# Optimization experiments

Measured on AMD Instinct MI355X. Metric: run time of the kernel, lower is better.

The kernel has to match this reference:

```python
import jax, jax.numpy as jnp
import numpy as np

CHUNK_SIZE = 64
EPS = 1e-6


def setup_inputs() -> dict:
    key = jax.random.key(0)
    ks = jax.random.split(key, 5)
    B, NH, S, DH = 2, 16, 4096, 64
    return {
        "q": jax.random.normal(ks[0], (B, NH, S, DH), dtype=jnp.float32),
        "k": jax.random.normal(ks[1], (B, NH, S, DH), dtype=jnp.float32),
        "v": jax.random.normal(ks[2], (B, NH, S, DH), dtype=jnp.float32),
        "igate_preact": jax.random.normal(ks[3], (B, NH, S), dtype=jnp.float32),
        "fgate_preact": jax.random.normal(ks[4], (B, NH, S), dtype=jnp.float32),
    }


def _mlstm_intra(q, k, v, ig, fg, chunk_size, eps):
    # q,k,v: [B,NH,S,DH]; ig,fg: [B,NH,S]
    B, NH, S, DH = q.shape
    L = chunk_size
    NC = S // L
    qc = q.reshape(B, NH, NC, L, DH)
    kc = k.reshape(B, NH, NC, L, DH)
    vc = v.reshape(B, NH, NC, L, DH)
    igc = ig.reshape(B, NH, NC, L)
    fgc = fg.reshape(B, NH, NC, L)

    # log forget gates and their within-chunk cumulative sums
    log_fg = jax.nn.log_sigmoid(fgc)                      # [B,NH,NC,L]
    log_fg_cum = jnp.cumsum(log_fg, axis=-1)              # [B,NH,NC,L]

    # gated decay matrix: logD[i,j] = sum_{t=j+1..i} log f_t + i_j  for j<=i
    log_fg_mat = log_fg_cum[..., :, None] - log_fg_cum[..., None, :]  # [B,NH,NC,L,L]
    log_D = log_fg_mat + igc[..., None, :]
    causal = jnp.tril(jnp.ones((L, L), dtype=bool))
    log_D = jnp.where(causal, log_D, -jnp.inf)

    # stabilizer (row-wise max)
    m = jnp.max(log_D, axis=-1)                           # [B,NH,NC,L]
    D = jnp.exp(log_D - m[..., None])                     # [B,NH,NC,L,L]

    # QK scores scaled, gated by decay matrix
    scale = 1.0 / jnp.sqrt(jnp.asarray(DH, dtype=q.dtype))
    scores = jnp.einsum("bncld,bncsd->bncls", qc, kc) * scale
    C = scores * D                                        # [B,NH,NC,L,L]

    # stabilized normalizer: max(|row sum|, exp(-m))
    n = jnp.maximum(jnp.abs(jnp.sum(C, axis=-1)), jnp.exp(-m))  # [B,NH,NC,L]
    h = jnp.einsum("bncls,bncsd->bncld", C, vc) / (n[..., None] + eps)
    return h.reshape(B, NH, S, DH)


def reference(q, k, v, igate_preact, fgate_preact):
    return _mlstm_intra(q, k, v, igate_preact, fgate_preact, CHUNK_SIZE, EPS)
```

## Files before the change

kernel.cpp:

```cpp
#include <hip/hip_runtime.h>
#include <hip/hip_bf16.h>
#include <math.h>

namespace {

typedef __bf16 bf16x8 __attribute__((ext_vector_type(8)));
typedef float f32x4 __attribute__((ext_vector_type(4)));

constexpr int L = 64;
constexpr int DH = 64;

__device__ __forceinline__ int kkey(int r) { return (r ^ (r >> 2)) & 7; }

__device__ __forceinline__ int swzV(int d, int j) {
  return d * 128 + ((((j >> 3) ^ kkey(d)) & 7) << 4) + (j & 7) * 2;
}
__device__ __forceinline__ int swzC(int r, int j) {
  return r * 128 + ((((j >> 3) ^ kkey(r)) & 7) << 4) + (j & 7) * 2;
}

__device__ __forceinline__ unsigned short bfbits(float f) {
  __bf16 h = (__bf16)f;
  return __builtin_bit_cast(unsigned short, h);
}
__device__ __forceinline__ __bf16 tobf(float f) { return (__bf16)f; }

__global__ __launch_bounds__(256) void mlstm_mfma(
    const float* __restrict__ q, const float* __restrict__ k,
    const float* __restrict__ v, const float* __restrict__ ig,
    const float* __restrict__ fg, float* __restrict__ out) {

  __shared__ __align__(16) char lds[8192 + 4 * 2048];
  __shared__ __align__(16) float ea_sh[64];
  __shared__ __align__(16) float eb_sh[64];
  __shared__ __align__(16) float em_sh[64];

  const int tid = threadIdx.x;
  const int w = tid >> 6;
  const int lane = tid & 63;
  const int m = lane & 15;
  const int g = lane >> 4;
  const size_t cbase = (size_t)blockIdx.x * (L * DH);
  const size_t gb = (size_t)blockIdx.x * L;

  const float4* v4 = (const float4*)(v + cbase);
  float4 vbuf[4];
#pragma unroll
  for (int it = 0; it < 4; ++it) vbuf[it] = v4[it * 256 + tid];

  float fgv = 0.f, igv = 0.f;
  if (w == 0) {
    fgv = fg[gb + lane];
    igv = ig[gb + lane];
  }

  bf16x8 qf[2];
#pragma unroll
  for (int kb = 0; kb < 2; ++kb) {
    const int off = (w * 16 + m) * 64 + kb * 32 + g * 8;
    const float4 q0 = *(const float4*)(q + cbase + off);
    const float4 q1 = *(const float4*)(q + cbase + off + 4);
    qf[kb] = bf16x8{tobf(q0.x), tobf(q0.y), tobf(q0.z), tobf(q0.w),
                    tobf(q1.x), tobf(q1.y), tobf(q1.z), tobf(q1.w)};
  }
  bf16x8 kf[4][2];
#pragma unroll
  for (int rb = 0; rb < 4; ++rb) {
    if (rb <= w) {
#pragma unroll
      for (int kb = 0; kb < 2; ++kb) {
        const int off = (rb * 16 + m) * 64 + kb * 32 + g * 8;
        const float4 k0 = *(const float4*)(k + cbase + off);
        const float4 k1 = *(const float4*)(k + cbase + off + 4);
        kf[rb][kb] = bf16x8{tobf(k0.x), tobf(k0.y), tobf(k0.z), tobf(k0.w),
                            tobf(k1.x), tobf(k1.y), tobf(k1.z), tobf(k1.w)};
      }
    }
  }

  if (w == 0) {
    const float lf = fminf(fgv, 0.f) - log1pf(__expf(-fabsf(fgv)));
    float cum = lf;
#pragma unroll
    for (int o = 1; o < 64; o <<= 1) {
      const float t = __shfl_up(cum, o, 64);
      if (lane >= o) cum += t;
    }
    const float a = igv - cum;
    float b = a;
#pragma unroll
    for (int o = 1; o < 64; o <<= 1) {
      const float t = __shfl_up(b, o, 64);
      if (lane >= o) b = fmaxf(b, t);
    }
    const float bmax = __shfl(b, 63, 64);
    ea_sh[lane] = 0.125f * __expf(a - bmax);
    eb_sh[lane] = __expf(bmax - b);
    em_sh[lane] = __expf(-(b + cum));
  }

  {
    unsigned short* vt = (unsigned short*)lds;
#pragma unroll
    for (int it = 0; it < 4; ++it) {
      const int idx = it * 256 + tid;
      const int j = idx >> 4;
      const int d0 = (idx & 15) * 4;
      vt[swzV(d0 + 0, j) >> 1] = bfbits(vbuf[it].x);
      vt[swzV(d0 + 1, j) >> 1] = bfbits(vbuf[it].y);
      vt[swzV(d0 + 2, j) >> 1] = bfbits(vbuf[it].z);
      vt[swzV(d0 + 3, j) >> 1] = bfbits(vbuf[it].w);
    }
  }

  __syncthreads();

  const int njb = (w >= 2) ? 2 : 1;
  bf16x8 vfr[4][2];
#pragma unroll
  for (int db = 0; db < 4; ++db)
#pragma unroll
    for (int jb = 0; jb < 2; ++jb)
      if (jb < njb)
        vfr[db][jb] =
            *(const bf16x8*)(lds + swzV(db * 16 + m, jb * 32 + g * 8));

  f32x4 st[4];
#pragma unroll
  for (int rb = 0; rb < 4; ++rb) {
    if (rb <= w) {
      f32x4 acc = {0.f, 0.f, 0.f, 0.f};
      acc = __builtin_amdgcn_mfma_f32_16x16x32_bf16(kf[rb][0], qf[0], acc, 0, 0, 0);
      acc = __builtin_amdgcn_mfma_f32_16x16x32_bf16(kf[rb][1], qf[1], acc, 0, 0, 0);
      st[rb] = acc;
    }
  }

  char* cw = lds + 8192 + w * 2048;
  const int i = w * 16 + m;
  const float ebv = eb_sh[i];
  float rs = 0.f;
  const int rbfill = w | 1;
#pragma unroll
  for (int rb = 0; rb < 4; ++rb) {
    if (rb <= rbfill) {
      unsigned long long wp = 0ull;
      if (rb <= w) {
        const float4 ea4 = *(const float4*)&ea_sh[rb * 16 + g * 4];
        const float eav[4] = {ea4.x, ea4.y, ea4.z, ea4.w};
#pragma unroll
        for (int e = 0; e < 4; ++e) {
          const int j = rb * 16 + g * 4 + e;
          const float val = (j <= i) ? st[rb][e] * eav[e] * ebv : 0.f;
          rs += val;
          wp |= (unsigned long long)bfbits(val) << (16 * e);
        }
      }
      *(unsigned long long*)(cw + swzC(m, rb * 16 + g * 4)) = wp;
    }
  }
  rs += __shfl_xor(rs, 16, 64);
  rs += __shfl_xor(rs, 32, 64);
  const float invv = 1.f / (fmaxf(fabsf(rs), em_sh[i]) + 1e-6f);

  const bf16x8 c0 = *(const bf16x8*)(cw + swzC(m, g * 8));
  f32x4 acc[4];
#pragma unroll
  for (int db = 0; db < 4; ++db) {
    f32x4 z = {0.f, 0.f, 0.f, 0.f};
    acc[db] = __builtin_amdgcn_mfma_f32_16x16x32_bf16(vfr[db][0], c0, z, 0, 0, 0);
  }
  if (w >= 2) {
    const bf16x8 c1 = *(const bf16x8*)(cw + swzC(m, 32 + g * 8));
#pragma unroll
    for (int db = 0; db < 4; ++db)
      acc[db] = __builtin_amdgcn_mfma_f32_16x16x32_bf16(vfr[db][1], c1, acc[db], 0, 0, 0);
  }

  float* op = out + cbase + i * 64 + g * 4;
#pragma unroll
  for (int db = 0; db < 4; ++db) {
    const f32x4 hv = acc[db];
    *(float4*)(op + db * 16) =
        make_float4(hv[0] * invv, hv[1] * invv, hv[2] * invv, hv[3] * invv);
  }
}

}

extern "C" void kernel_launch(void* const* d_in, const int* in_sizes, int n_in,
                              void* d_out, int out_size, void* d_ws,
                              size_t ws_size, hipStream_t stream) {
  const float* q = (const float*)d_in[0];
  const float* k = (const float*)d_in[1];
  const float* v = (const float*)d_in[2];
  const float* ig = (const float*)d_in[3];
  const float* fg = (const float*)d_in[4];
  float* out = (float*)d_out;

  const int total = in_sizes[0];
  const int nchunks = total / (L * DH);
  mlstm_mfma<<<dim3(nchunks), dim3(256), 0, stream>>>(q, k, v, ig, fg, out);
}
```

Before: 30.26 us.

## Remove block-wide sync by loading V fragments directly and computing gates per wave

Every wave now computes the gate scan redundantly and shares its per-row factors through lane shuffles instead of shared memory. V is loaded straight from global memory in fragment order, replacing the transposed LDS staging. Together these drop the block-wide __syncthreads and shrink LDS use, and launch bounds now request 4 blocks per CU. The cost is strided scalar global loads for V, redundant gate math in each wave, and more registers held for V values.

New measurement: 34.74 us. +14.8%, slower.

```diff
diff --git a/kernel.cpp b/kernel.cpp
--- a/kernel.cpp
+++ b/kernel.cpp
@@ -11,10 +11,6 @@
 constexpr int DH = 64;
 
 __device__ __forceinline__ int kkey(int r) { return (r ^ (r >> 2)) & 7; }
-
-__device__ __forceinline__ int swzV(int d, int j) {
-  return d * 128 + ((((j >> 3) ^ kkey(d)) & 7) << 4) + (j & 7) * 2;
-}
 __device__ __forceinline__ int swzC(int r, int j) {
   return r * 128 + ((((j >> 3) ^ kkey(r)) & 7) << 4) + (j & 7) * 2;
 }
@@ -25,15 +21,12 @@
 }
 __device__ __forceinline__ __bf16 tobf(float f) { return (__bf16)f; }
 
-__global__ __launch_bounds__(256) void mlstm_mfma(
+__global__ __launch_bounds__(256, 4) void mlstm_mfma(
     const float* __restrict__ q, const float* __restrict__ k,
     const float* __restrict__ v, const float* __restrict__ ig,
     const float* __restrict__ fg, float* __restrict__ out) {
 
-  __shared__ __align__(16) char lds[8192 + 4 * 2048];
-  __shared__ __align__(16) float ea_sh[64];
-  __shared__ __align__(16) float eb_sh[64];
-  __shared__ __align__(16) float em_sh[64];
+  __shared__ __align__(16) char lds[4 * 2048];
 
   const int tid = threadIdx.x;
   const int w = tid >> 6;
@@ -43,16 +36,21 @@
   const size_t cbase = (size_t)blockIdx.x * (L * DH);
   const size_t gb = (size_t)blockIdx.x * L;
 
-  const float4* v4 = (const float4*)(v + cbase);
-  float4 vbuf[4];
+  const float fgv = fg[gb + lane];
+  const float igv = ig[gb + lane];
+
+  const int njb = (w >= 2) ? 2 : 1;
+  float vtmp[4][2][8];
 #pragma unroll
-  for (int it = 0; it < 4; ++it) vbuf[it] = v4[it * 256 + tid];
-
-  float fgv = 0.f, igv = 0.f;
-  if (w == 0) {
-    fgv = fg[gb + lane];
-    igv = ig[gb + lane];
-  }
+  for (int db = 0; db < 4; ++db)
+#pragma unroll
+    for (int jb = 0; jb < 2; ++jb)
+      if (jb < njb) {
+        const float* vp =
+            v + cbase + (size_t)(jb * 32 + g * 8) * 64 + db * 16 + m;
+#pragma unroll
+        for (int t = 0; t < 8; ++t) vtmp[db][jb][t] = vp[t * 64];
+      }
 
   bf16x8 qf[2];
 #pragma unroll
@@ -78,7 +76,8 @@
     }
   }
 
-  if (w == 0) {
+  float ea, eb, em;
+  {
     const float lf = fminf(fgv, 0.f) - log1pf(__expf(-fabsf(fgv)));
     float cum = lf;
 #pragma unroll
@@ -94,36 +93,21 @@
       if (lane >= o) b = fmaxf(b, t);
     }
     const float bmax = __shfl(b, 63, 64);
-    ea_sh[lane] = 0.125f * __expf(a - bmax);
-    eb_sh[lane] = __expf(bmax - b);
-    em_sh[lane] = __expf(-(b + cum));
+    ea = 0.125f * __expf(a - bmax);
+    eb = __expf(bmax - b);
+    em = __expf(-(b + cum));
   }
 
-  {
-    unsigned short* vt = (unsigned short*)lds;
-#pragma unroll
-    for (int it = 0; it < 4; ++it) {
-      const int idx = it * 256 + tid;
-      const int j = idx >> 4;
-      const int d0 = (idx & 15) * 4;
-      vt[swzV(d0 + 0, j) >> 1] = bfbits(vbuf[it].x);
-      vt[swzV(d0 + 1, j) >> 1] = bfbits(vbuf[it].y);
-      vt[swzV(d0 + 2, j) >> 1] = bfbits(vbuf[it].z);
-      vt[swzV(d0 + 3, j) >> 1] = bfbits(vbuf[it].w);
-    }
-  }
-
-  __syncthreads();
-
-  const int njb = (w >= 2) ? 2 : 1;
   bf16x8 vfr[4][2];
 #pragma unroll
   for (int db = 0; db < 4; ++db)
 #pragma unroll
     for (int jb = 0; jb < 2; ++jb)
-      if (jb < njb)
-        vfr[db][jb] =
-            *(const bf16x8*)(lds + swzV(db * 16 + m, jb * 32 + g * 8));
+      if (jb < njb) {
+        const float* t = vtmp[db][jb];
+        vfr[db][jb] = bf16x8{tobf(t[0]), tobf(t[1]), tobf(t[2]), tobf(t[3]),
+                             tobf(t[4]), tobf(t[5]), tobf(t[6]), tobf(t[7])};
+      }
 
   f32x4 st[4];
 #pragma unroll
@@ -136,9 +120,10 @@
     }
   }
 
-  char* cw = lds + 8192 + w * 2048;
+  char* cw = lds + w * 2048;
   const int i = w * 16 + m;
-  const float ebv = eb_sh[i];
+  const float ebv = __shfl(eb, i, 64);
+  const float emv = __shfl(em, i, 64);
   float rs = 0.f;
   const int rbfill = w | 1;
 #pragma unroll
@@ -146,12 +131,11 @@
     if (rb <= rbfill) {
       unsigned long long wp = 0ull;
       if (rb <= w) {
-        const float4 ea4 = *(const float4*)&ea_sh[rb * 16 + g * 4];
-        const float eav[4] = {ea4.x, ea4.y, ea4.z, ea4.w};
 #pragma unroll
         for (int e = 0; e < 4; ++e) {
           const int j = rb * 16 + g * 4 + e;
-          const float val = (j <= i) ? st[rb][e] * eav[e] * ebv : 0.f;
+          const float eaj = __shfl(ea, j, 64);
+          const float val = (j <= i) ? st[rb][e] * eaj * ebv : 0.f;
           rs += val;
           wp |= (unsigned long long)bfbits(val) << (16 * e);
         }
@@ -161,7 +145,7 @@
   }
   rs += __shfl_xor(rs, 16, 64);
   rs += __shfl_xor(rs, 32, 64);
-  const float invv = 1.f / (fmaxf(fabsf(rs), em_sh[i]) + 1e-6f);
+  const float invv = 1.f / (fmaxf(fabsf(rs), emv) + 1e-6f);
 
   const bf16x8 c0 = *(const bf16x8*)(cw + swzC(m, g * 8));
   f32x4 acc[4];
```
